# Performance work log

Hardware: AMD Instinct MI355X
Metric: run time of the kernel (lower is better)

The kernel has to match this reference:

```python
import jax, jax.numpy as jnp
import numpy as np
import math

D_MODEL = 1024
NUM_HEADS = 16
B, L = 2, 2048
# scale_level=0, patch_time_span=1 -> effective_stride=1
PERIODS = (1.0, 30.0)
WEIGHTS = (0.8, 0.4)
SIGMAS = (0.5, 2.0)


def setup_inputs() -> dict:
    key = jax.random.key(0)
    ks = jax.random.split(key, 10)
    s = 1.0 / math.sqrt(D_MODEL)
    inp = {
        "x": jax.random.normal(ks[0], (B, L, D_MODEL), dtype=jnp.float32),
        "Wq": jax.random.normal(ks[1], (D_MODEL, D_MODEL), dtype=jnp.float32) * s,
        "bq": jax.random.normal(ks[2], (D_MODEL,), dtype=jnp.float32) * 0.01,
        "Wk": jax.random.normal(ks[3], (D_MODEL, D_MODEL), dtype=jnp.float32) * s,
        "bk": jax.random.normal(ks[4], (D_MODEL,), dtype=jnp.float32) * 0.01,
        "Wv": jax.random.normal(ks[5], (D_MODEL, D_MODEL), dtype=jnp.float32) * s,
        "bv": jax.random.normal(ks[6], (D_MODEL,), dtype=jnp.float32) * 0.01,
        "Wo": jax.random.normal(ks[7], (D_MODEL, D_MODEL), dtype=jnp.float32) * s,
        "bo": jax.random.normal(ks[8], (D_MODEL,), dtype=jnp.float32) * 0.01,
        "prior_lambda": jnp.asarray(2.0, dtype=jnp.float32),
    }
    return inp


def _gaussian_mask(length):
    idx = jnp.arange(length, dtype=jnp.float32)
    delta = jnp.abs(idx[:, None] - idx[None, :])  # [L, L]
    mask = jnp.zeros_like(delta)
    for p, w, sigma in zip(PERIODS, WEIGHTS, SIGMAS):
        if p < 0.2:
            continue
        mask = mask + w * jnp.exp(-((delta - p) ** 2) / (2.0 * sigma ** 2))
    return mask


def reference(x, Wq, bq, Wk, bk, Wv, bv, Wo, bo, prior_lambda):
    Bx, Lx, D = x.shape
    H = NUM_HEADS
    hd = D // H

    def split_heads(t):  # [B, L, D] -> [B, H, L, hd]
        return t.reshape(Bx, Lx, H, hd).transpose(0, 2, 1, 3)

    Q = split_heads(x @ Wq.T + bq)
    K = split_heads(x @ Wk.T + bk)
    V = split_heads(x @ Wv.T + bv)

    scores = jnp.einsum("bhqd,bhkd->bhqk", Q, K) / math.sqrt(hd)
    scores = scores + prior_lambda * _gaussian_mask(Lx)[None, None, :, :]
    attn = jax.nn.softmax(scores, axis=-1)
    out = jnp.einsum("bhqk,bhkd->bhqd", attn, V)
    out = out.transpose(0, 2, 1, 3).reshape(Bx, Lx, D)
    return out @ Wo.T + bo
```

## Files before the change

kernel.cpp:

```cpp
#include <hip/hip_runtime.h>

#define D_MODEL 1024
#define SEQ_L   2048
#define NHEADS  16
#define HDIM    64
#define NROWS   4096

#define QSCALE 0.18033688011112042f
#define LOG2E  1.4426950408889634f

#if __has_builtin(__builtin_amdgcn_exp2f)
#define EXP2F(x) __builtin_amdgcn_exp2f(x)
#else
#define EXP2F(x) __expf((x) * 0.6931471805599453f)
#endif

typedef __attribute__((ext_vector_type(8))) short short8;
typedef __attribute__((ext_vector_type(4))) short short4v;
typedef __attribute__((ext_vector_type(4))) float floatx4;
typedef __attribute__((ext_vector_type(4))) unsigned short ushort4v;
typedef unsigned short ushort;

static __device__ __forceinline__ ushort f2bf(float f) {
    unsigned int u = __float_as_uint(f);
    u += 0x7FFFu + ((u >> 16) & 1u);
    return (ushort)(u >> 16);
}

static __device__ __forceinline__ floatx4 mfma16(short8 a, short8 b, floatx4 c) {
    return __builtin_amdgcn_mfma_f32_16x16x32_bf16(a, b, c, 0, 0, 0);
}

static __device__ __forceinline__ floatx4 mfma16k16(short4v a, short4v b, floatx4 c) {
    return __builtin_amdgcn_mfma_f32_16x16x16bf16_1k(a, b, c, 0, 0, 0);
}

static __device__ __forceinline__ void store8bf(ushort* dst, float4 a, float4 b) {
    uint4 pk;
    pk.x = (unsigned)f2bf(a.x) | ((unsigned)f2bf(a.y) << 16);
    pk.y = (unsigned)f2bf(a.z) | ((unsigned)f2bf(a.w) << 16);
    pk.z = (unsigned)f2bf(b.x) | ((unsigned)f2bf(b.y) << 16);
    pk.w = (unsigned)f2bf(b.z) | ((unsigned)f2bf(b.w) << 16);
    *(uint4*)dst = pk;
}

static __device__ __forceinline__ void gll16(const ushort* g, ushort* l) {
    __builtin_amdgcn_global_load_lds(
        (const __attribute__((address_space(1))) unsigned int*)(const unsigned int*)g,
        (__attribute__((address_space(3))) unsigned int*)(unsigned int*)l,
        16, 0, 0);
}

__global__ __launch_bounds__(256) void convert_bf16(
    const float* __restrict__ x,
    const float* __restrict__ wq, const float* __restrict__ wk,
    const float* __restrict__ wv, const float* __restrict__ wo,
    ushort* __restrict__ xb, ushort* __restrict__ wb3, ushort* __restrict__ wob)
{
    const int seg = blockIdx.y;
    const float* src;
    ushort* dst;
    int n;
    if      (seg == 0) { src = x;  dst = xb;                n = 4194304; }
    else if (seg == 1) { src = wq; dst = wb3;               n = 1048576; }
    else if (seg == 2) { src = wk; dst = wb3 + 1048576;     n = 1048576; }
    else if (seg == 3) { src = wv; dst = wb3 + 2097152;     n = 1048576; }
    else               { src = wo; dst = wob;               n = 1048576; }
    const int i = (blockIdx.x * 256 + threadIdx.x) * 8;
    if (i >= n) return;
    float4 a = *(const float4*)(src + i);
    float4 b = *(const float4*)(src + i + 4);
    store8bf(dst + i, a, b);
}

__global__ __launch_bounds__(256, 4) void gemm_qkv(
    const ushort* __restrict__ A, const ushort* __restrict__ B,
    const float* __restrict__ bq, const float* __restrict__ bk,
    const float* __restrict__ bv,
    ushort* __restrict__ Qo, ushort* __restrict__ Ko, ushort* __restrict__ Vo)
{
    __shared__ ushort As[64 * 64];
    __shared__ ushort Bs[128 * 64];

    const int tid  = threadIdx.x;
    const int w    = tid >> 6;
    const int lane = tid & 63;
    const int l15  = lane & 15;
    const int quad = lane >> 4;

    const int bm = blockIdx.y * 64;
    const int bn = blockIdx.x * 128;
    const int z  = blockIdx.x >> 3;

    const int ciA0 = tid,        ciA1 = tid + 256;
    const int rA0 = ciA0 >> 3,   rA1 = ciA1 >> 3;
    const int sA0i = ciA0 & 7,   sA1i = ciA1 & 7;
    const ushort* aP0 = A + (size_t)(bm + rA0) * 1024 + (sA0i ^ (rA0 & 7)) * 8;
    const ushort* aP1 = A + (size_t)(bm + rA1) * 1024 + (sA1i ^ (rA1 & 7)) * 8;
    ushort* lA0 = &As[rA0 * 64 + sA0i * 8];
    ushort* lA1 = &As[rA1 * 64 + sA1i * 8];

    const ushort* bP[4];
    ushort* lB[4];
#pragma unroll
    for (int p = 0; p < 4; p++) {
        const int ci = tid + p * 256;
        const int r = ci >> 3, s = ci & 7;
        bP[p] = B + (size_t)(bn + r) * 1024 + (s ^ (r & 7)) * 8;
        lB[p] = &Bs[r * 64 + s * 8];
    }

    const int x7 = l15 & 7;

    floatx4 acc[4][2];
#pragma unroll
    for (int i = 0; i < 4; i++)
#pragma unroll
        for (int j = 0; j < 2; j++) acc[i][j] = (floatx4){0.f, 0.f, 0.f, 0.f};

    for (int k0 = 0; k0 < 1024; k0 += 64) {
        __syncthreads();
        gll16(aP0 + k0, lA0);
        gll16(aP1 + k0, lA1);
#pragma unroll
        for (int p = 0; p < 4; p++) gll16(bP[p] + k0, lB[p]);
        __syncthreads();

#pragma unroll
        for (int kk = 0; kk < 2; kk++) {
            const int slot = ((kk * 4 + quad) ^ x7) * 8;
            short8 af[4], bf[2];
#pragma unroll
            for (int mi = 0; mi < 4; mi++)
                af[mi] = *(const short8*)&As[(mi * 16 + l15) * 64 + slot];
#pragma unroll
            for (int ni = 0; ni < 2; ni++)
                bf[ni] = *(const short8*)&Bs[(w * 32 + ni * 16 + l15) * 64 + slot];
            if (z == 2) {
#pragma unroll
                for (int mi = 0; mi < 4; mi++)
#pragma unroll
                    for (int ni = 0; ni < 2; ni++)
                        acc[mi][ni] = mfma16(af[mi], bf[ni], acc[mi][ni]);
            } else {
#pragma unroll
                for (int mi = 0; mi < 4; mi++)
#pragma unroll
                    for (int ni = 0; ni < 2; ni++)
                        acc[mi][ni] = mfma16(bf[ni], af[mi], acc[mi][ni]);
            }
        }
    }

    const int cwbase = bn & 1023;
    if (z == 2) {
#pragma unroll
        for (int ni = 0; ni < 2; ni++) {
            const int within = cwbase + w * 32 + ni * 16 + l15;
            const int h  = within >> 6;
            const int hd = within & 63;
            const float bvl = bv[within];
#pragma unroll
            for (int mi = 0; mi < 4; mi++) {
                const int row = bm + mi * 16 + quad * 4;
                const int bb = row >> 11, li = row & 2047;
                ushort4v pk;
#pragma unroll
                for (int r = 0; r < 4; r++) pk[r] = f2bf(acc[mi][ni][r] + bvl);
                *(ushort4v*)(Vo + ((size_t)(bb * NHEADS + h) * HDIM + hd) * SEQ_L + li) = pk;
            }
        }
    } else {
        const float* bias = z ? bk : bq;
        const float scale = z ? 1.0f : QSCALE;
        ushort* outp = z ? Ko : Qo;
#pragma unroll
        for (int ni = 0; ni < 2; ni++) {
            const int colw = cwbase + w * 32 + ni * 16 + quad * 4;
            const int h   = colw >> 6;
            const int hd0 = colw & 63;
            const float4 bb4 = *(const float4*)&bias[colw];
#pragma unroll
            for (int mi = 0; mi < 4; mi++) {
                const int row = bm + mi * 16 + l15;
                const int bb = row >> 11, li = row & 2047;
                ushort4v pk;
                pk[0] = f2bf((acc[mi][ni][0] + bb4.x) * scale);
                pk[1] = f2bf((acc[mi][ni][1] + bb4.y) * scale);
                pk[2] = f2bf((acc[mi][ni][2] + bb4.z) * scale);
                pk[3] = f2bf((acc[mi][ni][3] + bb4.w) * scale);
                *(ushort4v*)(outp + ((size_t)(bb * NHEADS + h) * SEQ_L + li) * HDIM + hd0) = pk;
            }
        }
    }
}

__global__ __launch_bounds__(256, 4) void attn(
    const ushort* __restrict__ Q,
    const ushort* __restrict__ K,
    const ushort* __restrict__ Vt,
    const float* __restrict__ lam,
    ushort* __restrict__ O0, ushort* __restrict__ O1,
    float* __restrict__ Lw)
{
    __shared__ float mtab[128];
    __shared__ ushort Ks[2][64 * 64];
    __shared__ ushort Vts[2][64 * 64];

    const int tid  = threadIdx.x;
    const int wave = tid >> 6;
    const int lane = tid & 63;
    const int l15  = lane & 15;
    const int quad = lane >> 4;

    const int qb = blockIdx.x;
    const int h  = blockIdx.y;
    const int zz = blockIdx.z;
    const int bz = zz >> 1;
    const int sp = zz & 1;
    const int bh = bz * NHEADS + h;
    const int q0 = qb * 128;
    const int kb = sp * 1024;

    const float lambda = *lam;
    if (tid < 128) {
        float d  = (float)tid;
        float e1 = (d - 1.f) * (d - 1.f);
        float e2 = (d - 30.f) * (d - 30.f);
        mtab[tid] = LOG2E * lambda *
                    (0.8f * __expf(-2.0f * e1) + 0.4f * __expf(-0.125f * e2));
    }

    const ushort* qp =
        Q + ((size_t)bh * SEQ_L + q0 + wave * 16 + l15) * HDIM + quad * 8;
    short8 qf[2][2];
    qf[0][0] = *(const short8*)qp;
    qf[0][1] = *(const short8*)(qp + 32);
    qf[1][0] = *(const short8*)(qp + 64 * HDIM);
    qf[1][1] = *(const short8*)(qp + 64 * HDIM + 32);

    const ushort* kbase = K  + ((size_t)bh * SEQ_L) * HDIM;
    const ushort* vbase = Vt + ((size_t)bh * HDIM) * SEQ_L;

    const int cid0 = tid, cid1 = 256 + tid;
    const int row0 = cid0 >> 3, row1 = cid1 >> 3;
    const int cl0  = (cid0 & 7) ^ (row0 & 7);
    const int cl1  = (cid1 & 7) ^ (row1 & 7);
    const ushort* kg0 = kbase + (size_t)(kb + row0) * HDIM + cl0 * 8;
    const ushort* kg1 = kbase + (size_t)(kb + row1) * HDIM + cl1 * 8;
    const ushort* vg0 = vbase + (size_t)row0 * SEQ_L + kb + cl0 * 8;
    const ushort* vg1 = vbase + (size_t)row1 * SEQ_L + kb + cl1 * 8;

    floatx4 o[2][4];
#pragma unroll
    for (int g = 0; g < 2; g++)
#pragma unroll
        for (int i = 0; i < 4; i++) o[g][i] = (floatx4){0.f, 0.f, 0.f, 0.f};
    floatx4 ol[2];
    ol[0] = (floatx4){0.f, 0.f, 0.f, 0.f};
    ol[1] = (floatx4){0.f, 0.f, 0.f, 0.f};

    short4v ones;
    ones[0] = 0x3F80; ones[1] = 0x3F80; ones[2] = 0x3F80; ones[3] = 0x3F80;

    gll16(kg0, &Ks[0][cid0 * 8]);
    gll16(kg1, &Ks[0][cid1 * 8]);
    gll16(vg0, &Vts[0][cid0 * 8]);
    gll16(vg1, &Vts[0][cid1 * 8]);

    const int xo = l15 & 7;

    for (int t = 0; t < 16; t++) {
        const int cur = t & 1;
        __syncthreads();
        if (t + 1 < 16) {
            const int nxt = cur ^ 1;
            const int koff = (t + 1) * 64;
            gll16(kg0 + (size_t)koff * HDIM, &Ks[nxt][cid0 * 8]);
            gll16(kg1 + (size_t)koff * HDIM, &Ks[nxt][cid1 * 8]);
            gll16(vg0 + koff, &Vts[nxt][cid0 * 8]);
            gll16(vg1 + koff, &Vts[nxt][cid1 * 8]);
        }

        floatx4 s[2][4];
#pragma unroll
        for (int g = 0; g < 2; g++)
#pragma unroll
            for (int i = 0; i < 4; i++) s[g][i] = (floatx4){0.f, 0.f, 0.f, 0.f};
#pragma unroll
        for (int kk = 0; kk < 2; kk++) {
#pragma unroll
            for (int nt = 0; nt < 4; nt++) {
                const int slot = (kk * 4 + quad) ^ xo;
                short8 kf = *(const short8*)&Ks[cur][(nt * 16 + l15) * 64 + slot * 8];
                s[0][nt] = mfma16(kf, qf[0][kk], s[0][nt]);
                s[1][nt] = mfma16(kf, qf[1][kk], s[1][nt]);
            }
        }

        const int j = sp * 16 + t;
#pragma unroll
        for (int g = 0; g < 2; g++) {
            const int tg = j - (qb * 2 + g);
            if (tg >= -1 && tg <= 1) {
                const int qg = q0 + g * 64 + wave * 16 + l15;
#pragma unroll
                for (int nt = 0; nt < 4; nt++) {
                    const int kgi = j * 64 + nt * 16 + quad * 4;
#pragma unroll
                    for (int r = 0; r < 4; r++) {
                        int dq = qg - (kgi + r);
                        int ad = dq < 0 ? -dq : dq;
                        s[g][nt][r] += mtab[ad];
                    }
                }
            }
        }

        short4v pb[2][4];
#pragma unroll
        for (int g = 0; g < 2; g++) {
#pragma unroll
            for (int nt = 0; nt < 4; nt++) {
                unsigned ur[4];
#pragma unroll
                for (int r = 0; r < 4; r++)
                    ur[r] = __float_as_uint(EXP2F(s[g][nt][r])) + 0x8000u;
                uint2 pk;
                pk.x = __builtin_amdgcn_perm(ur[1], ur[0], 0x07060302u);
                pk.y = __builtin_amdgcn_perm(ur[3], ur[2], 0x07060302u);
                pb[g][nt] = __builtin_bit_cast(short4v, pk);
            }
        }

#pragma unroll
        for (int kc = 0; kc < 4; kc++) {
#pragma unroll
            for (int nt = 0; nt < 4; nt++) {
                const int slot = (2 * kc + (quad >> 1)) ^ xo;
                short4v vf = *(const short4v*)
                    &Vts[cur][(nt * 16 + l15) * 64 + slot * 8 + (quad & 1) * 4];
                o[0][nt] = mfma16k16(vf, pb[0][kc], o[0][nt]);
                o[1][nt] = mfma16k16(vf, pb[1][kc], o[1][nt]);
            }
            ol[0] = mfma16k16(ones, pb[0][kc], ol[0]);
            ol[1] = mfma16k16(ones, pb[1][kc], ol[1]);
        }
    }

    ushort* Osp = sp ? O1 : O0;
#pragma unroll
    for (int g = 0; g < 2; g++) {
        const int qg = q0 + g * 64 + wave * 16 + l15;
        if (quad == 0)
            Lw[((size_t)(sp * 2 + bz) * NHEADS + h) * SEQ_L + qg] = ol[g][0];
        ushort* obase = Osp + ((size_t)bz * SEQ_L + qg) * D_MODEL + h * HDIM;
#pragma unroll
        for (int nt = 0; nt < 4; nt++) {
            ushort4v pk;
#pragma unroll
            for (int r = 0; r < 4; r++) pk[r] = f2bf(o[g][nt][r]);
            *(ushort4v*)(obase + nt * 16 + quad * 4) = pk;
        }
    }
}

__global__ __launch_bounds__(256) void merge_attn(
    const ushort* __restrict__ O0, const ushort* __restrict__ O1,
    const float* __restrict__ Lw, ushort* __restrict__ Aout)
{
    const int gid = blockIdx.x * 256 + threadIdx.x;
    const int i = gid * 8;
    const int row = i >> 10;
    const int h   = (i >> 6) & 15;
    const int bz  = row >> 11, q = row & 2047;
    const int li  = (bz * NHEADS + h) * SEQ_L + q;
    const float linv = 1.f / (Lw[li] + Lw[2 * NHEADS * SEQ_L + li]);

    uint4 a = *(const uint4*)(O0 + i);
    uint4 b = *(const uint4*)(O1 + i);
    unsigned aw[4] = {a.x, a.y, a.z, a.w};
    unsigned bw[4] = {b.x, b.y, b.z, b.w};
    uint4 res;
    unsigned rw[4];
#pragma unroll
    for (int k = 0; k < 4; k++) {
        float alo = __uint_as_float(aw[k] << 16);
        float ahi = __uint_as_float(aw[k] & 0xFFFF0000u);
        float blo = __uint_as_float(bw[k] << 16);
        float bhi = __uint_as_float(bw[k] & 0xFFFF0000u);
        float lo = (alo + blo) * linv;
        float hi = (ahi + bhi) * linv;
        rw[k] = (unsigned)f2bf(lo) | ((unsigned)f2bf(hi) << 16);
    }
    res.x = rw[0]; res.y = rw[1]; res.z = rw[2]; res.w = rw[3];
    *(uint4*)(Aout + i) = res;
}

__global__ __launch_bounds__(256, 4) void gemm_out(
    const ushort* __restrict__ A, const ushort* __restrict__ B,
    const float* __restrict__ bo, float* __restrict__ out)
{
    __shared__ ushort As[64 * 64];
    __shared__ ushort Bs[64 * 64];

    const int tid  = threadIdx.x;
    const int w    = tid >> 6;
    const int lane = tid & 63;
    const int l15  = lane & 15;
    const int quad = lane >> 4;

    const int bm = blockIdx.y * 64;
    const int bn = blockIdx.x * 64;

    const int ci0 = tid, ci1 = tid + 256;
    const int r0 = ci0 >> 3, r1 = ci1 >> 3;
    const int s0 = ci0 & 7,  s1 = ci1 & 7;
    const ushort* aP0 = A + (size_t)(bm + r0) * 1024 + (s0 ^ (r0 & 7)) * 8;
    const ushort* aP1 = A + (size_t)(bm + r1) * 1024 + (s1 ^ (r1 & 7)) * 8;
    const ushort* bP0 = B + (size_t)(bn + r0) * 1024 + (s0 ^ (r0 & 7)) * 8;
    const ushort* bP1 = B + (size_t)(bn + r1) * 1024 + (s1 ^ (r1 & 7)) * 8;
    ushort* lA0 = &As[r0 * 64 + s0 * 8];
    ushort* lA1 = &As[r1 * 64 + s1 * 8];
    ushort* lB0 = &Bs[r0 * 64 + s0 * 8];
    ushort* lB1 = &Bs[r1 * 64 + s1 * 8];

    const int x7 = l15 & 7;

    floatx4 acc[4];
#pragma unroll
    for (int i = 0; i < 4; i++) acc[i] = (floatx4){0.f, 0.f, 0.f, 0.f};

    for (int k0 = 0; k0 < 1024; k0 += 64) {
        __syncthreads();
        gll16(aP0 + k0, lA0);
        gll16(aP1 + k0, lA1);
        gll16(bP0 + k0, lB0);
        gll16(bP1 + k0, lB1);
        __syncthreads();

#pragma unroll
        for (int kk = 0; kk < 2; kk++) {
            const int slot = ((kk * 4 + quad) ^ x7) * 8;
            short8 bf = *(const short8*)&Bs[(w * 16 + l15) * 64 + slot];
#pragma unroll
            for (int mi = 0; mi < 4; mi++) {
                short8 af = *(const short8*)&As[(mi * 16 + l15) * 64 + slot];
                acc[mi] = mfma16(bf, af, acc[mi]);
            }
        }
    }

    const int col0 = bn + w * 16 + quad * 4;
    const float4 bb4 = *(const float4*)&bo[col0];
#pragma unroll
    for (int mi = 0; mi < 4; mi++) {
        const int row = bm + mi * 16 + l15;
        float4 st;
        st.x = acc[mi][0] + bb4.x;
        st.y = acc[mi][1] + bb4.y;
        st.z = acc[mi][2] + bb4.z;
        st.w = acc[mi][3] + bb4.w;
        *(float4*)(out + (size_t)row * 1024 + col0) = st;
    }
}

extern "C" void kernel_launch(void* const* d_in, const int* in_sizes, int n_in,
                              void* d_out, int out_size, void* d_ws, size_t ws_size,
                              hipStream_t stream)
{
    const float* x   = (const float*)d_in[0];
    const float* Wq  = (const float*)d_in[1];
    const float* bq  = (const float*)d_in[2];
    const float* Wk  = (const float*)d_in[3];
    const float* bk  = (const float*)d_in[4];
    const float* Wv  = (const float*)d_in[5];
    const float* bv  = (const float*)d_in[6];
    const float* Wo  = (const float*)d_in[7];
    const float* bo  = (const float*)d_in[8];
    const float* lam = (const float*)d_in[9];
    float* out = (float*)d_out;

    const size_t NELEM = (size_t)NROWS * D_MODEL;
    ushort* Qw  = (ushort*)d_ws;
    ushort* Kw  = Qw + NELEM;
    ushort* Vw  = Kw + NELEM;
    ushort* O0  = Vw + NELEM;
    ushort* O1  = O0 + NELEM;
    ushort* XA  = O1 + NELEM;
    ushort* Wb3 = XA + NELEM;
    ushort* Wob = Wb3 + 3 * 1024 * 1024;
    float*  Lw  = (float*)(Wob + 1024 * 1024);

    dim3 gc(2048, 5);
    convert_bf16<<<gc, 256, 0, stream>>>(x, Wq, Wk, Wv, Wo, XA, Wb3, Wob);

    dim3 g1(3072 / 128, NROWS / 64);
    gemm_qkv<<<g1, 256, 0, stream>>>(XA, Wb3, bq, bk, bv, Qw, Kw, Vw);

    dim3 g2(SEQ_L / 128, NHEADS, 4);
    attn<<<g2, 256, 0, stream>>>(Qw, Kw, Vw, lam, O0, O1, Lw);

    merge_attn<<<NELEM / (256 * 8), 256, 0, stream>>>(O0, O1, Lw, XA);

    dim3 g3(1024 / 64, NROWS / 64);
    gemm_out<<<g3, 256, 0, stream>>>(XA, Wob, bo, out);
}
```

Before: 199.2 us.

## Fuse x conversion into QKV GEMM and split-merge into output GEMM

The separate fp32-to-bf16 conversion of x and the merge_attn kernel are removed. The QKV GEMM now loads fp32 x directly and converts it while staging into LDS. The output GEMM combines the two split-K attention partials and their normalisers while loading its A tile. This removes two kernel launches and the global round-trips of the intermediate bf16 buffers. The cost is that fp32 x is re-read by every N-tile block (24x), merge arithmetic is repeated across 16 column blocks, and the A loads are now synchronous register loads instead of direct-to-LDS transfers.

```diff
diff --git a/kernel.cpp b/kernel.cpp
--- a/kernel.cpp
+++ b/kernel.cpp
@@ -51,30 +51,23 @@
         16, 0, 0);
 }
 
-__global__ __launch_bounds__(256) void convert_bf16(
-    const float* __restrict__ x,
+__global__ __launch_bounds__(256) void convert_w(
     const float* __restrict__ wq, const float* __restrict__ wk,
     const float* __restrict__ wv, const float* __restrict__ wo,
-    ushort* __restrict__ xb, ushort* __restrict__ wb3, ushort* __restrict__ wob)
+    ushort* __restrict__ wb3, ushort* __restrict__ wob)
 {
-    const int seg = blockIdx.y;
-    const float* src;
-    ushort* dst;
-    int n;
-    if      (seg == 0) { src = x;  dst = xb;                n = 4194304; }
-    else if (seg == 1) { src = wq; dst = wb3;               n = 1048576; }
-    else if (seg == 2) { src = wk; dst = wb3 + 1048576;     n = 1048576; }
-    else if (seg == 3) { src = wv; dst = wb3 + 2097152;     n = 1048576; }
-    else               { src = wo; dst = wob;               n = 1048576; }
     const int i = (blockIdx.x * 256 + threadIdx.x) * 8;
-    if (i >= n) return;
-    float4 a = *(const float4*)(src + i);
-    float4 b = *(const float4*)(src + i + 4);
-    store8bf(dst + i, a, b);
+    const int seg = i >> 20;
+    const int within = i & 1048575;
+    const float* src = (seg == 0) ? wq : (seg == 1) ? wk : (seg == 2) ? wv : wo;
+    ushort* dst = (seg < 3) ? (wb3 + i) : (wob + within);
+    float4 a = *(const float4*)(src + within);
+    float4 b = *(const float4*)(src + within + 4);
+    store8bf(dst, a, b);
 }
 
 __global__ __launch_bounds__(256, 4) void gemm_qkv(
-    const ushort* __restrict__ A, const ushort* __restrict__ B,
+    const float* __restrict__ X, const ushort* __restrict__ B,
     const float* __restrict__ bq, const float* __restrict__ bk,
     const float* __restrict__ bv,
     ushort* __restrict__ Qo, ushort* __restrict__ Ko, ushort* __restrict__ Vo)
@@ -92,13 +85,13 @@
     const int bn = blockIdx.x * 128;
     const int z  = blockIdx.x >> 3;
 
-    const int ciA0 = tid,        ciA1 = tid + 256;
-    const int rA0 = ciA0 >> 3,   rA1 = ciA1 >> 3;
-    const int sA0i = ciA0 & 7,   sA1i = ciA1 & 7;
-    const ushort* aP0 = A + (size_t)(bm + rA0) * 1024 + (sA0i ^ (rA0 & 7)) * 8;
-    const ushort* aP1 = A + (size_t)(bm + rA1) * 1024 + (sA1i ^ (rA1 & 7)) * 8;
-    ushort* lA0 = &As[rA0 * 64 + sA0i * 8];
-    ushort* lA1 = &As[rA1 * 64 + sA1i * 8];
+    const int ciA0 = tid, ciA1 = tid + 256;
+    const int rA0 = ciA0 >> 3, rA1 = ciA1 >> 3;
+    const int sA0 = ciA0 & 7,  sA1 = ciA1 & 7;
+    const float* axP0 = X + (size_t)(bm + rA0) * 1024 + (sA0 ^ (rA0 & 7)) * 8;
+    const float* axP1 = X + (size_t)(bm + rA1) * 1024 + (sA1 ^ (rA1 & 7)) * 8;
+    ushort* lA0 = &As[rA0 * 64 + sA0 * 8];
+    ushort* lA1 = &As[rA1 * 64 + sA1 * 8];
 
     const ushort* bP[4];
     ushort* lB[4];
@@ -120,10 +113,14 @@
 
     for (int k0 = 0; k0 < 1024; k0 += 64) {
         __syncthreads();
-        gll16(aP0 + k0, lA0);
-        gll16(aP1 + k0, lA1);
 #pragma unroll
         for (int p = 0; p < 4; p++) gll16(bP[p] + k0, lB[p]);
+        float4 fa00 = *(const float4*)(axP0 + k0);
+        float4 fa01 = *(const float4*)(axP0 + k0 + 4);
+        float4 fa10 = *(const float4*)(axP1 + k0);
+        float4 fa11 = *(const float4*)(axP1 + k0 + 4);
+        store8bf(lA0, fa00, fa01);
+        store8bf(lA1, fa10, fa11);
         __syncthreads();
 
 #pragma unroll
@@ -365,40 +362,10 @@
     }
 }
 
-__global__ __launch_bounds__(256) void merge_attn(
+__global__ __launch_bounds__(256, 4) void gemm_out(
     const ushort* __restrict__ O0, const ushort* __restrict__ O1,
-    const float* __restrict__ Lw, ushort* __restrict__ Aout)
-{
-    const int gid = blockIdx.x * 256 + threadIdx.x;
-    const int i = gid * 8;
-    const int row = i >> 10;
-    const int h   = (i >> 6) & 15;
-    const int bz  = row >> 11, q = row & 2047;
-    const int li  = (bz * NHEADS + h) * SEQ_L + q;
-    const float linv = 1.f / (Lw[li] + Lw[2 * NHEADS * SEQ_L + li]);
-
-    uint4 a = *(const uint4*)(O0 + i);
-    uint4 b = *(const uint4*)(O1 + i);
-    unsigned aw[4] = {a.x, a.y, a.z, a.w};
-    unsigned bw[4] = {b.x, b.y, b.z, b.w};
-    uint4 res;
-    unsigned rw[4];
-#pragma unroll
-    for (int k = 0; k < 4; k++) {
-        float alo = __uint_as_float(aw[k] << 16);
-        float ahi = __uint_as_float(aw[k] & 0xFFFF0000u);
-        float blo = __uint_as_float(bw[k] << 16);
-        float bhi = __uint_as_float(bw[k] & 0xFFFF0000u);
-        float lo = (alo + blo) * linv;
-        float hi = (ahi + bhi) * linv;
-        rw[k] = (unsigned)f2bf(lo) | ((unsigned)f2bf(hi) << 16);
-    }
-    res.x = rw[0]; res.y = rw[1]; res.z = rw[2]; res.w = rw[3];
-    *(uint4*)(Aout + i) = res;
-}
-
-__global__ __launch_bounds__(256, 4) void gemm_out(
-    const ushort* __restrict__ A, const ushort* __restrict__ B,
+    const float* __restrict__ Lw,
+    const ushort* __restrict__ B,
     const float* __restrict__ bo, float* __restrict__ out)
 {
     __shared__ ushort As[64 * 64];
@@ -412,14 +379,22 @@
 
     const int bm = blockIdx.y * 64;
     const int bn = blockIdx.x * 64;
+    const int bz = bm >> 11;
+    const int NL = 2 * NHEADS * SEQ_L;
 
     const int ci0 = tid, ci1 = tid + 256;
     const int r0 = ci0 >> 3, r1 = ci1 >> 3;
     const int s0 = ci0 & 7,  s1 = ci1 & 7;
-    const ushort* aP0 = A + (size_t)(bm + r0) * 1024 + (s0 ^ (r0 & 7)) * 8;
-    const ushort* aP1 = A + (size_t)(bm + r1) * 1024 + (s1 ^ (r1 & 7)) * 8;
-    const ushort* bP0 = B + (size_t)(bn + r0) * 1024 + (s0 ^ (r0 & 7)) * 8;
-    const ushort* bP1 = B + (size_t)(bn + r1) * 1024 + (s1 ^ (r1 & 7)) * 8;
+    const int c0 = (s0 ^ (r0 & 7)) * 8;
+    const int c1 = (s1 ^ (r1 & 7)) * 8;
+    const ushort* o0P0 = O0 + (size_t)(bm + r0) * 1024 + c0;
+    const ushort* o0P1 = O0 + (size_t)(bm + r1) * 1024 + c1;
+    const ushort* o1P0 = O1 + (size_t)(bm + r0) * 1024 + c0;
+    const ushort* o1P1 = O1 + (size_t)(bm + r1) * 1024 + c1;
+    const int liB0 = bz * NHEADS * SEQ_L + ((bm + r0) & 2047);
+    const int liB1 = bz * NHEADS * SEQ_L + ((bm + r1) & 2047);
+    const ushort* bP0 = B + (size_t)(bn + r0) * 1024 + c0;
+    const ushort* bP1 = B + (size_t)(bn + r1) * 1024 + c1;
     ushort* lA0 = &As[r0 * 64 + s0 * 8];
     ushort* lA1 = &As[r1 * 64 + s1 * 8];
     ushort* lB0 = &Bs[r0 * 64 + s0 * 8];
@@ -433,10 +408,53 @@
 
     for (int k0 = 0; k0 < 1024; k0 += 64) {
         __syncthreads();
-        gll16(aP0 + k0, lA0);
-        gll16(aP1 + k0, lA1);
         gll16(bP0 + k0, lB0);
         gll16(bP1 + k0, lB1);
+
+        const int hoff = (k0 >> 6) * SEQ_L;
+        const float linv0 = __builtin_amdgcn_rcpf(
+            Lw[liB0 + hoff] + Lw[NL + liB0 + hoff]);
+        const float linv1 = __builtin_amdgcn_rcpf(
+            Lw[liB1 + hoff] + Lw[NL + liB1 + hoff]);
+
+        uint4 a0 = *(const uint4*)(o0P0 + k0);
+        uint4 b0 = *(const uint4*)(o1P0 + k0);
+        uint4 a1 = *(const uint4*)(o0P1 + k0);
+        uint4 b1 = *(const uint4*)(o1P1 + k0);
+
+        uint4 res0, res1;
+        {
+            unsigned aw[4] = {a0.x, a0.y, a0.z, a0.w};
+            unsigned bw[4] = {b0.x, b0.y, b0.z, b0.w};
+            unsigned rw[4];
+#pragma unroll
+            for (int k = 0; k < 4; k++) {
+                float lo = (__uint_as_float(aw[k] << 16) +
+                            __uint_as_float(bw[k] << 16)) * linv0;
+                float hi = (__uint_as_float(aw[k] & 0xFFFF0000u) +
+                            __uint_as_float(bw[k] & 0xFFFF0000u)) * linv0;
+                rw[k] = ((__float_as_uint(lo) + 0x8000u) >> 16) |
+                        ((__float_as_uint(hi) + 0x8000u) & 0xFFFF0000u);
+            }
+            res0.x = rw[0]; res0.y = rw[1]; res0.z = rw[2]; res0.w = rw[3];
+        }
+        {
+            unsigned aw[4] = {a1.x, a1.y, a1.z, a1.w};
+            unsigned bw[4] = {b1.x, b1.y, b1.z, b1.w};
+            unsigned rw[4];
+#pragma unroll
+            for (int k = 0; k < 4; k++) {
+                float lo = (__uint_as_float(aw[k] << 16) +
+                            __uint_as_float(bw[k] << 16)) * linv1;
+                float hi = (__uint_as_float(aw[k] & 0xFFFF0000u) +
+                            __uint_as_float(bw[k] & 0xFFFF0000u)) * linv1;
+                rw[k] = ((__float_as_uint(lo) + 0x8000u) >> 16) |
+                        ((__float_as_uint(hi) + 0x8000u) & 0xFFFF0000u);
+            }
+            res1.x = rw[0]; res1.y = rw[1]; res1.z = rw[2]; res1.w = rw[3];
+        }
+        *(uint4*)lA0 = res0;
+        *(uint4*)lA1 = res1;
         __syncthreads();
 
 #pragma unroll
@@ -487,22 +505,18 @@
     ushort* Vw  = Kw + NELEM;
     ushort* O0  = Vw + NELEM;
     ushort* O1  = O0 + NELEM;
-    ushort* XA  = O1 + NELEM;
-    ushort* Wb3 = XA + NELEM;
+    ushort* Wb3 = O1 + NELEM;
     ushort* Wob = Wb3 + 3 * 1024 * 1024;
     float*  Lw  = (float*)(Wob + 1024 * 1024);
 
-    dim3 gc(2048, 5);
-    convert_bf16<<<gc, 256, 0, stream>>>(x, Wq, Wk, Wv, Wo, XA, Wb3, Wob);
+    convert_w<<<2048, 256, 0, stream>>>(Wq, Wk, Wv, Wo, Wb3, Wob);
 
     dim3 g1(3072 / 128, NROWS / 64);
-    gemm_qkv<<<g1, 256, 0, stream>>>(XA, Wb3, bq, bk, bv, Qw, Kw, Vw);
+    gemm_qkv<<<g1, 256, 0, stream>>>(x, Wb3, bq, bk, bv, Qw, Kw, Vw);
 
     dim3 g2(SEQ_L / 128, NHEADS, 4);
     attn<<<g2, 256, 0, stream>>>(Qw, Kw, Vw, lam, O0, O1, Lw);
 
-    merge_attn<<<NELEM / (256 * 8), 256, 0, stream>>>(O0, O1, Lw, XA);
-
     dim3 g3(1024 / 64, NROWS / 64);
-    gemm_out<<<g3, 256, 0, stream>>>(XA, Wob, bo, out);
-}
+    gemm_out<<<g3, 256, 0, stream>>>(O0, O1, Lw, Wob, bo, out);
+}
```

New measurement: 227.8 us. 1.14x slower.
